# Performance work log

Measured on AMD Instinct MI355X. Metric: run time of the kernel, lower is better.

The kernel has to match this reference:

```python
import jax, jax.numpy as jnp
import numpy as np

B, S, D_MODEL, N_HEADS, D_K, D_V = 2, 2048, 1024, 16, 64, 64


def setup_inputs() -> dict:
    key = jax.random.key(0)
    k1, k2, k3, k4, k5, k6, k7 = jax.random.split(key, 7)
    scale = 1.0 / np.sqrt(D_MODEL)
    inputs = {
        "input_Q": jax.random.normal(k1, (B, S, D_MODEL), dtype=jnp.float32),
        "input_K": jax.random.normal(k2, (B, S, D_MODEL), dtype=jnp.float32),
        "input_V": jax.random.normal(k3, (B, S, D_MODEL), dtype=jnp.float32),
        # causal mask: True means position is masked out (matches masked_fill_)
        "attn_mask": jnp.broadcast_to(
            ~jnp.tril(jnp.ones((S, S), dtype=bool)), (B, S, S)
        ),
        "flag": 0,
        "W_Q": jax.random.normal(k4, (D_MODEL, N_HEADS * D_K), dtype=jnp.float32) * scale,
        "W_K": jax.random.normal(k5, (D_MODEL, N_HEADS * D_K), dtype=jnp.float32) * scale,
        "W_V": jax.random.normal(k6, (D_MODEL, N_HEADS * D_V), dtype=jnp.float32) * scale,
        "W_O": jax.random.normal(k7, (N_HEADS * D_V, D_MODEL), dtype=jnp.float32) * scale,
    }
    return inputs


def reference(input_Q, input_K, input_V, attn_mask, flag, W_Q, W_K, W_V, W_O):
    b = input_Q.shape[0]
    # project and split heads: [b, h, s, d]
    Q = (input_Q @ W_Q).reshape(b, -1, N_HEADS, D_K).transpose(0, 2, 1, 3)
    K = (input_K @ W_K).reshape(b, -1, N_HEADS, D_K).transpose(0, 2, 1, 3)
    V = (input_V @ W_V).reshape(b, -1, N_HEADS, D_V).transpose(0, 2, 1, 3)
    # scaled dot-product attention with additive large-negative masking
    scores = jnp.einsum("bhqd,bhkd->bhqk", Q, K) / np.sqrt(D_K).astype(np.float32)
    scores = jnp.where(attn_mask[:, None, :, :], jnp.float32(-1e9), scores)
    attn = jax.nn.softmax(scores, axis=-1)
    context = jnp.einsum("bhqk,bhkd->bhqd", attn, V)  # [b, h, s, d_v]
    context = context.transpose(0, 2, 1, 3).reshape(b, -1, N_HEADS * D_V)
    return context @ W_O
```

## Files before the change

kernel.cpp:

```cpp
#include <hip/hip_runtime.h>

#define DEVINL __device__ __forceinline__

typedef __attribute__((ext_vector_type(8))) short short8;
typedef __attribute__((ext_vector_type(4))) short sh4;
typedef __attribute__((ext_vector_type(4))) float floatx4;

constexpr int S_LEN = 2048;
constexpr int DM    = 1024;
constexpr int NHEAD = 16;
constexpr int DHEAD = 64;
constexpr int BATCH = 2;
constexpr int MROWS = BATCH * S_LEN;
constexpr float LOG2E = 1.44269504f;
constexpr float SM_C1 = 0.125f * LOG2E;
constexpr float SM_C2 = -24.0f * LOG2E;

#define MFMA16(a, b, c) __builtin_amdgcn_mfma_f32_16x16x16bf16_1k(a, b, c, 0, 0, 0)

DEVINL unsigned short f2bf(float x) {
  union { float f; unsigned u; } un; un.f = x;
  unsigned u = un.u;
  return (unsigned short)((u + 0x7fffu + ((u >> 16) & 1u)) >> 16);
}
DEVINL unsigned short f2bf_fast(float x) {
  union { float f; unsigned u; } un; un.f = x;
  return (unsigned short)((un.u + 0x8000u) >> 16);
}

__global__ __launch_bounds__(256) void prep_kernel(const float* __restrict__ s0,
                                                   const float* __restrict__ s1,
                                                   const float* __restrict__ s2,
                                                   unsigned short* __restrict__ d0,
                                                   unsigned short* __restrict__ d1,
                                                   unsigned short* __restrict__ d2,
                                                   const float* __restrict__ W0,
                                                   const float* __restrict__ W1,
                                                   const float* __restrict__ W2,
                                                   const float* __restrict__ W3,
                                                   unsigned short* __restrict__ T0,
                                                   unsigned short* __restrict__ T1,
                                                   unsigned short* __restrict__ T2,
                                                   unsigned short* __restrict__ T3) {
  __shared__ unsigned short tile[32][33];
  const int y = blockIdx.y;
  if (y < 3) {
    const float* s = y == 0 ? s0 : (y == 1 ? s1 : s2);
    unsigned short* d = y == 0 ? d0 : (y == 1 ? d1 : d2);
    int i = (blockIdx.x * 256 + threadIdx.x) * 4;
    float4 v = *(const float4*)(s + i);
    unsigned lo = (unsigned)f2bf(v.x) | ((unsigned)f2bf(v.y) << 16);
    unsigned hi = (unsigned)f2bf(v.z) | ((unsigned)f2bf(v.w) << 16);
    *(uint2*)(d + i) = make_uint2(lo, hi);
  } else {
    const int x = blockIdx.x;
    const int wsel = x >> 10, rem = x & 1023;
    const float* W = wsel == 0 ? W0 : (wsel == 1 ? W1 : (wsel == 2 ? W2 : W3));
    unsigned short* Wt = wsel == 0 ? T0 : (wsel == 1 ? T1 : (wsel == 2 ? T2 : T3));
    int t = threadIdx.x;
    int c = t & 31, r0 = t >> 5;
    int nB = (rem & 31) * 32, kB = (rem >> 5) * 32;
    for (int i = 0; i < 4; ++i) {
      int r = r0 + i * 8;
      tile[r][c] = f2bf(W[(size_t)(kB + r) * DM + nB + c]);
    }
    __syncthreads();
    for (int i = 0; i < 4; ++i) {
      int r = r0 + i * 8;
      Wt[(size_t)(nB + r) * DM + kB + c] = tile[c][r];
    }
  }
}

DEVINL void load_lds16(const unsigned short* g, unsigned short* l) {
  __builtin_amdgcn_global_load_lds((const __attribute__((address_space(1))) unsigned int*)g,
                                   (__attribute__((address_space(3))) unsigned int*)l,
                                   16, 0, 0);
}

template <int MODE>
DEVINL void gemm_body(const unsigned short* __restrict__ A,
                      const unsigned short* __restrict__ Bt,
                      void* __restrict__ Cout) {
  constexpr int K = 1024, N = 1024;
  __shared__ alignas(16) unsigned short As[128 * 32];
  __shared__ alignas(16) unsigned short Bs[128 * 32];
  const int tid  = threadIdx.x;
  const int wave = tid >> 6, lane = tid & 63;
  const int quad = lane >> 4, l16 = lane & 15;
  const int mBase = blockIdx.y * 128, nBase = blockIdx.x * 128;
  const int wm = (wave >> 1) * 64, wn = (wave & 1) * 64;
  const int sr = lane >> 2;
  const int sc = (lane & 3) * 8;
  floatx4 acc[4][4] = {};

  for (int k0 = 0; k0 < K; k0 += 32) {
    __syncthreads();
#pragma unroll
    for (int j = 0; j < 2; ++j) {
      int row = wave * 32 + j * 16 + sr;
      load_lds16(A  + (size_t)(mBase + row) * K + k0 + sc, As + (wave * 32 + j * 16) * 32);
      load_lds16(Bt + (size_t)(nBase + row) * K + k0 + sc, Bs + (wave * 32 + j * 16) * 32);
    }
    __syncthreads();
    short8 af[4], bfr[4];
#pragma unroll
    for (int mt = 0; mt < 4; ++mt) af[mt]  = *(const short8*)&As[(wm + mt * 16 + l16) * 32 + quad * 8];
#pragma unroll
    for (int nt = 0; nt < 4; ++nt) bfr[nt] = *(const short8*)&Bs[(wn + nt * 16 + l16) * 32 + quad * 8];
#pragma unroll
    for (int mt = 0; mt < 4; ++mt)
#pragma unroll
      for (int nt = 0; nt < 4; ++nt)
        acc[mt][nt] = __builtin_amdgcn_mfma_f32_16x16x32_bf16(af[mt], bfr[nt], acc[mt][nt], 0, 0, 0);
  }

#pragma unroll
  for (int mt = 0; mt < 4; ++mt)
#pragma unroll
    for (int nt = 0; nt < 4; ++nt) {
      const int m = mBase + wm + mt * 16 + quad * 4;
      const int n = nBase + wn + nt * 16 + l16;
      if (MODE == 2) {
        const int bq = m >> 11, s = m & 2047;
        const int hh = n >> 6,  d = n & 63;
        unsigned short w4[4];
#pragma unroll
        for (int r = 0; r < 4; ++r) w4[r] = f2bf(acc[mt][nt][r]);
        *(uint2*)&((unsigned short*)Cout)[((size_t)((bq * 16 + hh) * 64 + d)) * S_LEN + s] =
            *(const uint2*)w4;
      } else {
#pragma unroll
        for (int r = 0; r < 4; ++r)
          ((unsigned short*)Cout)[(size_t)(m + r) * N + n] = f2bf(acc[mt][nt][r]);
      }
    }
}

__global__ __launch_bounds__(256) void gemm_qkv(const unsigned short* __restrict__ A0,
                                                const unsigned short* __restrict__ A1,
                                                const unsigned short* __restrict__ A2,
                                                const unsigned short* __restrict__ B0,
                                                const unsigned short* __restrict__ B1,
                                                const unsigned short* __restrict__ B2,
                                                unsigned short* __restrict__ C0,
                                                unsigned short* __restrict__ C1,
                                                unsigned short* __restrict__ C2) {
  const int z = blockIdx.z;
  if (z == 2)      gemm_body<2>(A2, B2, C2);
  else if (z == 1) gemm_body<0>(A1, B1, C1);
  else             gemm_body<0>(A0, B0, C0);
}

__global__ __launch_bounds__(256) void gemm_out64(const unsigned short* __restrict__ A,
                                                  const unsigned short* __restrict__ Bt,
                                                  float* __restrict__ C) {
  constexpr int K = 1024, N = 1024;
  __shared__ alignas(16) unsigned short As[64 * 32];
  __shared__ alignas(16) unsigned short Bs[128 * 32];
  const int tid  = threadIdx.x;
  const int wave = tid >> 6, lane = tid & 63;
  const int quad = lane >> 4, l16 = lane & 15;
  const int mBase = blockIdx.y * 64, nBase = blockIdx.x * 128;
  const int wm = (wave >> 1) * 32, wn = (wave & 1) * 64;
  const int sr = lane >> 2;
  const int sc = (lane & 3) * 8;
  floatx4 acc[2][4] = {};

  for (int k0 = 0; k0 < K; k0 += 32) {
    __syncthreads();
    load_lds16(A + (size_t)(mBase + wave * 16 + sr) * K + k0 + sc, As + (wave * 16) * 32);
#pragma unroll
    for (int j = 0; j < 2; ++j) {
      int row = wave * 32 + j * 16 + sr;
      load_lds16(Bt + (size_t)(nBase + row) * K + k0 + sc, Bs + (wave * 32 + j * 16) * 32);
    }
    __syncthreads();
    short8 af[2], bfr[4];
#pragma unroll
    for (int mt = 0; mt < 2; ++mt) af[mt]  = *(const short8*)&As[(wm + mt * 16 + l16) * 32 + quad * 8];
#pragma unroll
    for (int nt = 0; nt < 4; ++nt) bfr[nt] = *(const short8*)&Bs[(wn + nt * 16 + l16) * 32 + quad * 8];
#pragma unroll
    for (int mt = 0; mt < 2; ++mt)
#pragma unroll
      for (int nt = 0; nt < 4; ++nt)
        acc[mt][nt] = __builtin_amdgcn_mfma_f32_16x16x32_bf16(af[mt], bfr[nt], acc[mt][nt], 0, 0, 0);
  }

#pragma unroll
  for (int mt = 0; mt < 2; ++mt)
#pragma unroll
    for (int nt = 0; nt < 4; ++nt)
#pragma unroll
      for (int r = 0; r < 4; ++r) {
        int m = mBase + wm + mt * 16 + quad * 4 + r;
        int n = nBase + wn + nt * 16 + l16;
        C[(size_t)m * N + n] = acc[mt][nt][r];
      }
}

__global__ __launch_bounds__(256, 3) void attn_kernel(const unsigned short* __restrict__ Qp,
                                                      const unsigned short* __restrict__ Kp,
                                                      const unsigned short* __restrict__ Vtg,
                                                      unsigned short* __restrict__ ctx) {
  const int lin = (int)blockIdx.y * 16 + (int)blockIdx.x;
  const int xcd = lin & 7;
  const int kk  = lin >> 3;
  const int bh  = ((kk >> 4) << 3) | xcd;
  const int pairIdx = kk & 15;
  const int b  = bh >> 4, h = bh & 15;
  const int tid = threadIdx.x;
  const int w = tid >> 6, lane = tid & 63;
  const int quad = lane >> 4, l16 = lane & 15;

  __shared__ alignas(16) unsigned short KVs[2 * 8192];
  __shared__ float rsL[4][4][16];
  __shared__ alignas(16) float Ored[4][4][16][20];

  const unsigned short* Kbh = Kp  + (size_t)(b * S_LEN) * DM + h * DHEAD;
  const unsigned short* Vbh = Vtg + (size_t)(bh * DHEAD) * S_LEN;

  int srow[4], scol[4];
#pragma unroll
  for (int j = 0; j < 4; ++j) {
    const int p = (w & 1) * 256 + j * 64 + lane;
    srow[j] = p >> 3;
    scol[j] = ((p & 7) ^ (srow[j] & 7)) * 8;
  }
  const bool stageK = (w < 2);

  const int swz = l16 & 7;
  const int kRow = (w * 16 + l16) * 64;
  const int kOff0 = kRow + ((0 + quad) ^ swz) * 8;
  const int kOff1 = kRow + ((4 + quad) ^ swz) * 8;
  int vOff[4];
#pragma unroll
  for (int dt = 0; dt < 4; ++dt) {
    const int ch = 2 * w + (quad >> 1);
    vOff[dt] = 4096 + (dt * 16 + l16) * 64 + (ch ^ swz) * 8 + (quad & 1) * 4;
  }

  {
    unsigned short* dst = KVs + w * 2048;
#pragma unroll
    for (int j = 0; j < 4; ++j) {
      const unsigned short* src = stageK
          ? Kbh + (size_t)srow[j] * DM + scol[j]
          : Vbh + (size_t)srow[j] * S_LEN + scol[j];
      load_lds16(src, dst + j * 512);
    }
  }

  int cur = 0;

#pragma unroll 1
  for (int half = 0; half < 2; ++half) {
    const int qt = half ? pairIdx : 31 - pairIdx;
    const int Q0 = qt * 64;
    const int nT = qt + 1;

    short8 qB[4][2];
#pragma unroll
    for (int nt = 0; nt < 4; ++nt) {
      const size_t qr = ((size_t)(b * S_LEN + Q0 + nt * 16 + l16)) * DM + h * DHEAD + quad * 8;
      qB[nt][0] = *(const short8*)&Qp[qr];
      qB[nt][1] = *(const short8*)&Qp[qr + 32];
    }

    floatx4 o[4][4] = {};
    float rs[4] = {0.f, 0.f, 0.f, 0.f};

#pragma unroll 1
    for (int t = 0; t < nT; ++t) {
      asm volatile("s_waitcnt vmcnt(0)" ::: "memory");
      __syncthreads();

      const unsigned short* buf = KVs + cur * 8192;
      short8 kc0 = *(const short8*)&buf[kOff0];
      short8 kc1 = *(const short8*)&buf[kOff1];
      sh4 vv[4];
#pragma unroll
      for (int dt = 0; dt < 4; ++dt) vv[dt] = *(const sh4*)&buf[vOff[dt]];

      {
        const int tn = (t + 1 < nT) ? t + 1 : 0;
        const int kb = tn * 64;
        unsigned short* dst = KVs + (cur ^ 1) * 8192 + w * 2048;
#pragma unroll
        for (int j = 0; j < 4; ++j) {
          const unsigned short* src = stageK
              ? Kbh + (size_t)(kb + srow[j]) * DM + scol[j]
              : Vbh + (size_t)srow[j] * S_LEN + kb + scol[j];
          load_lds16(src, dst + j * 512);
        }
      }

      const bool masked = (t == nT - 1);
      const int sbase = w * 16 + quad * 4;

#pragma unroll
      for (int nt = 0; nt < 4; ++nt) {
        floatx4 sc = {};
        sc = __builtin_amdgcn_mfma_f32_16x16x32_bf16(kc0, qB[nt][0], sc, 0, 0, 0);
        sc = __builtin_amdgcn_mfma_f32_16x16x32_bf16(kc1, qB[nt][1], sc, 0, 0, 0);
        const int qoff = nt * 16 + l16;
        sh4 pa;
        float acc = 0.f;
#pragma unroll
        for (int r = 0; r < 4; ++r) {
          float p = __builtin_amdgcn_exp2f(fmaf(sc[r], SM_C1, SM_C2));
          if (masked && (sbase + r > qoff)) p = 0.f;
          acc += p;
          pa[r] = (short)f2bf_fast(p);
        }
        rs[nt] += acc;
#pragma unroll
        for (int dt = 0; dt < 4; ++dt)
          o[nt][dt] = MFMA16(pa, vv[dt], o[nt][dt]);
      }

      cur ^= 1;
    }

#pragma unroll
    for (int nt = 0; nt < 4; ++nt) {
      rs[nt] += __shfl_xor(rs[nt], 16, 64);
      rs[nt] += __shfl_xor(rs[nt], 32, 64);
    }
    if (quad == 0) {
#pragma unroll
      for (int nt = 0; nt < 4; ++nt) rsL[w][nt][l16] = rs[nt];
    }

    for (int nt = 0; nt < 4; ++nt) {
      __syncthreads();
#pragma unroll
      for (int dt = 0; dt < 4; ++dt)
        *(floatx4*)&Ored[w][dt][l16][quad * 4] = o[nt][dt];
      __syncthreads();
      floatx4 acc = {};
#pragma unroll
      for (int w2 = 0; w2 < 4; ++w2) {
        floatx4 v = *(const floatx4*)&Ored[w2][w][l16][quad * 4];
#pragma unroll
        for (int j = 0; j < 4; ++j) acc[j] += v[j];
      }
#pragma unroll
      for (int j = 0; j < 4; ++j) {
        const int q16 = quad * 4 + j;
        float l = rsL[0][nt][q16] + rsL[1][nt][q16] + rsL[2][nt][q16] + rsL[3][nt][q16];
        const size_t row = (size_t)(b * S_LEN + Q0 + nt * 16 + q16);
        ctx[row * DM + h * DHEAD + w * 16 + l16] = f2bf(acc[j] / l);
      }
    }
  }
}

extern "C" void kernel_launch(void* const* d_in, const int* in_sizes, int n_in,
                              void* d_out, int out_size, void* d_ws, size_t ws_size,
                              hipStream_t stream) {
  const float* Xq = (const float*)d_in[0];
  const float* Xk = (const float*)d_in[1];
  const float* Xv = (const float*)d_in[2];
  const float* Wq = (const float*)d_in[5];
  const float* Wk = (const float*)d_in[6];
  const float* Wv = (const float*)d_in[7];
  const float* Wo = (const float*)d_in[8];
  float* out = (float*)d_out;

  char* ws = (char*)d_ws;
  constexpr size_t XBYTES = (size_t)MROWS * DM * 2;
  constexpr size_t WBYTES = (size_t)DM * DM * 2;
  unsigned short* xq_bf = (unsigned short*)(ws);
  unsigned short* xk_bf = (unsigned short*)(ws + XBYTES);
  unsigned short* xv_bf = (unsigned short*)(ws + 2 * XBYTES);
  unsigned short* wqt   = (unsigned short*)(ws + 3 * XBYTES);
  unsigned short* wkt   = (unsigned short*)(ws + 3 * XBYTES + WBYTES);
  unsigned short* wvt   = (unsigned short*)(ws + 3 * XBYTES + 2 * WBYTES);
  unsigned short* wot   = (unsigned short*)(ws + 3 * XBYTES + 3 * WBYTES);
  unsigned short* qp    = (unsigned short*)(ws + 3 * XBYTES + 4 * WBYTES);
  unsigned short* kp    = (unsigned short*)(ws + 4 * XBYTES + 4 * WBYTES);
  unsigned short* vt    = (unsigned short*)(ws + 5 * XBYTES + 4 * WBYTES);
  unsigned short* ctx   = xq_bf;

  prep_kernel<<<dim3(4096, 4), 256, 0, stream>>>(Xq, Xk, Xv, xq_bf, xk_bf, xv_bf,
                                                 Wq, Wk, Wv, Wo, wqt, wkt, wvt, wot);

  gemm_qkv<<<dim3(DM / 128, MROWS / 128, 3), 256, 0, stream>>>(
      xq_bf, xk_bf, xv_bf, wqt, wkt, wvt, qp, kp, vt);

  attn_kernel<<<dim3(16, BATCH * NHEAD), 256, 0, stream>>>(qp, kp, vt, ctx);

  gemm_out64<<<dim3(DM / 128, MROWS / 64), 256, 0, stream>>>(ctx, wot, out);
}
```

Before: 229.7 us.

## Triple-buffer K/V tiles across both query halves and reduce output via LDS atomics

Replaces the double-buffered K/V LDS staging with a three-buffer ring whose prefetch index runs continuously across both query-tile halves. Each step waits only for the older tile's loads (vmcnt(4)) and uses a raw s_barrier, so one tile's global loads stay in flight during compute. The cross-wave output reduction now zeroes a small shared accumulator and adds into it with LDS float atomics instead of writing a per-wave staging array and summing it. This frees LDS for the third buffer and removes the idle load latency at half boundaries. The cost is more LDS per block, which may lower occupancy, plus extra barriers and atomic contention in the epilogue.

Result: slower. 311.7 us (+35.7%).

```diff
diff --git a/kernel.cpp b/kernel.cpp
--- a/kernel.cpp
+++ b/kernel.cpp
@@ -214,9 +214,9 @@
   const int w = tid >> 6, lane = tid & 63;
   const int quad = lane >> 4, l16 = lane & 15;
 
-  __shared__ alignas(16) unsigned short KVs[2 * 8192];
+  __shared__ alignas(16) unsigned short KVs[3 * 8192];
+  __shared__ alignas(16) float Acc[4][16][20];
   __shared__ float rsL[4][4][16];
-  __shared__ alignas(16) float Ored[4][4][16][20];
 
   const unsigned short* Kbh = Kp  + (size_t)(b * S_LEN) * DM + h * DHEAD;
   const unsigned short* Vbh = Vtg + (size_t)(bh * DHEAD) * S_LEN;
@@ -241,24 +241,34 @@
     vOff[dt] = 4096 + (dt * 16 + l16) * 64 + (ch ^ swz) * 8 + (quad & 1) * 4;
   }
 
-  {
-    unsigned short* dst = KVs + w * 2048;
+  const int nT0 = 32 - pairIdx;
+  const int nT1 = pairIdx + 1;
+
+  auto kbOf = [&](int g) -> int {
+    if (g < nT0) return g * 64;
+    const int gg = g - nT0;
+    return (gg < nT1) ? gg * 64 : 0;
+  };
+  auto issueTile = [&](int kb, int wbuf) {
+    unsigned short* dst = KVs + wbuf * 8192 + w * 2048;
 #pragma unroll
     for (int j = 0; j < 4; ++j) {
       const unsigned short* src = stageK
-          ? Kbh + (size_t)srow[j] * DM + scol[j]
-          : Vbh + (size_t)srow[j] * S_LEN + scol[j];
+          ? Kbh + (size_t)(kb + srow[j]) * DM + scol[j]
+          : Vbh + (size_t)srow[j] * S_LEN + kb + scol[j];
       load_lds16(src, dst + j * 512);
     }
-  }
-
-  int cur = 0;
+  };
+
+  issueTile(kbOf(0), 0);
+  issueTile(kbOf(1), 1);
+  int rb = 0, wb = 2, g = 0;
 
 #pragma unroll 1
   for (int half = 0; half < 2; ++half) {
     const int qt = half ? pairIdx : 31 - pairIdx;
     const int Q0 = qt * 64;
-    const int nT = qt + 1;
+    const int nT = half ? nT1 : nT0;
 
     short8 qB[4][2];
 #pragma unroll
@@ -273,28 +283,19 @@
 
 #pragma unroll 1
     for (int t = 0; t < nT; ++t) {
-      asm volatile("s_waitcnt vmcnt(0)" ::: "memory");
-      __syncthreads();
-
-      const unsigned short* buf = KVs + cur * 8192;
+      asm volatile("s_waitcnt vmcnt(4)" ::: "memory");
+      __builtin_amdgcn_sched_barrier(0);
+      __builtin_amdgcn_s_barrier();
+      __builtin_amdgcn_sched_barrier(0);
+
+      const unsigned short* buf = KVs + rb * 8192;
       short8 kc0 = *(const short8*)&buf[kOff0];
       short8 kc1 = *(const short8*)&buf[kOff1];
       sh4 vv[4];
 #pragma unroll
       for (int dt = 0; dt < 4; ++dt) vv[dt] = *(const sh4*)&buf[vOff[dt]];
 
-      {
-        const int tn = (t + 1 < nT) ? t + 1 : 0;
-        const int kb = tn * 64;
-        unsigned short* dst = KVs + (cur ^ 1) * 8192 + w * 2048;
-#pragma unroll
-        for (int j = 0; j < 4; ++j) {
-          const unsigned short* src = stageK
-              ? Kbh + (size_t)(kb + srow[j]) * DM + scol[j]
-              : Vbh + (size_t)srow[j] * S_LEN + kb + scol[j];
-          load_lds16(src, dst + j * 512);
-        }
-      }
+      issueTile(kbOf(g + 2), wb);
 
       const bool masked = (t == nT - 1);
       const int sbase = w * 16 + quad * 4;
@@ -320,7 +321,9 @@
           o[nt][dt] = MFMA16(pa, vv[dt], o[nt][dt]);
       }
 
-      cur ^= 1;
+      rb = (rb == 2) ? 0 : rb + 1;
+      wb = (wb == 2) ? 0 : wb + 1;
+      ++g;
     }
 
 #pragma unroll
@@ -333,25 +336,28 @@
       for (int nt = 0; nt < 4; ++nt) rsL[w][nt][l16] = rs[nt];
     }
 
+#pragma unroll
     for (int nt = 0; nt < 4; ++nt) {
       __syncthreads();
+      {
+        float* af = &Acc[0][0][0];
+#pragma unroll
+        for (int z = 0; z < 5; ++z) af[tid * 5 + z] = 0.f;
+      }
+      __syncthreads();
 #pragma unroll
       for (int dt = 0; dt < 4; ++dt)
-        *(floatx4*)&Ored[w][dt][l16][quad * 4] = o[nt][dt];
+#pragma unroll
+        for (int j = 0; j < 4; ++j)
+          atomicAdd(&Acc[dt][l16][quad * 4 + j], o[nt][dt][j]);
       __syncthreads();
-      floatx4 acc = {};
-#pragma unroll
-      for (int w2 = 0; w2 < 4; ++w2) {
-        floatx4 v = *(const floatx4*)&Ored[w2][w][l16][quad * 4];
-#pragma unroll
-        for (int j = 0; j < 4; ++j) acc[j] += v[j];
-      }
 #pragma unroll
       for (int j = 0; j < 4; ++j) {
         const int q16 = quad * 4 + j;
-        float l = rsL[0][nt][q16] + rsL[1][nt][q16] + rsL[2][nt][q16] + rsL[3][nt][q16];
+        const float l = rsL[0][nt][q16] + rsL[1][nt][q16] +
+                        rsL[2][nt][q16] + rsL[3][nt][q16];
         const size_t row = (size_t)(b * S_LEN + Q0 + nt * 16 + q16);
-        ctx[row * DM + h * DHEAD + w * 16 + l16] = f2bf(acc[j] / l);
+        ctx[row * DM + h * DHEAD + w * 16 + l16] = f2bf(Acc[w][l16][q16] / l);
       }
     }
   }
```
